# Performance work log

Hardware: AMD Instinct MI355X
Metric: run time of the kernel (lower is better)

Reference implementation:

```python
import jax, jax.numpy as jnp
import numpy as np

B = 65536
D = 512
R = 64  # min(64, D) reflections (cap_householder_refl=True)


def setup_inputs() -> dict:
    key = jax.random.key(0)
    k1, k2 = jax.random.split(key)
    x = jax.random.normal(k1, (B, D), dtype=jnp.float32)
    sldj = jnp.zeros((B,), dtype=jnp.float32)
    householder_params = jax.random.normal(k2, (D, R), dtype=jnp.float32)
    return {"x": x, "sldj": sldj, "householder_params": householder_params}


def reference(x, sldj, householder_params):
    # Sequential Householder reflections: x <- x - 2 (x . u_hat) u_hat
    # params: (D, R); unconditioned, so u is shared across the batch.
    us = householder_params.T  # (R, D), scanned in forward order i = 0..R-1

    def step(xc, u):
        unit_u = u / jnp.linalg.norm(u)          # (D,)
        scalar = xc @ unit_u                      # (B,)
        xc = xc - 2.0 * scalar[:, None] * unit_u  # rank-1 update
        return xc, None

    out, _ = jax.lax.scan(step, x, us)
    return out, sldj
```

## Files before the change

### kernel.cpp

```cpp
#include <hip/hip_runtime.h>

typedef __attribute__((ext_vector_type(8))) short bf16x8;
typedef __attribute__((ext_vector_type(4))) float f32x4;

#define DD 512
#define RR 64
#define BTOT 65536
#define BM 64
#define BK 32

static __device__ __forceinline__ unsigned short f2bf(float f) {
    union { float f; unsigned u; } v; v.f = f;
    unsigned r = v.u + 0x7fffu + ((v.u >> 16) & 1u);
    return (unsigned short)(r >> 16);
}

__global__ void normalize_kernel(const float* __restrict__ P, float* __restrict__ U) {
    int i = blockIdx.x;
    int t = threadIdx.x;
    __shared__ float red[4];
    float a = P[t * RR + i];
    float b = P[(t + 256) * RR + i];
    float p = a * a + b * b;
#pragma unroll
    for (int off = 32; off > 0; off >>= 1) p += __shfl_down(p, off);
    if ((t & 63) == 0) red[t >> 6] = p;
    __syncthreads();
    float s = red[0] + red[1] + red[2] + red[3];
    float inv = 1.0f / sqrtf(s);
    U[i * DD + t]       = a * inv;
    U[i * DD + t + 256] = b * inv;
}

__global__ void compose_kernel(const float* __restrict__ U, unsigned short* __restrict__ Mt) {
    int k = blockIdx.x;
    int t = threadIdx.x;
    __shared__ float red[4];
    float v0 = (k < 256 && t == k) ? 1.0f : 0.0f;
    float v1 = (k >= 256 && t == (k - 256)) ? 1.0f : 0.0f;
    for (int i = 0; i < RR; ++i) {
        float u0 = U[i * DD + t];
        float u1 = U[i * DD + t + 256];
        float p = v0 * u0 + v1 * u1;
#pragma unroll
        for (int off = 32; off > 0; off >>= 1) p += __shfl_down(p, off);
        if ((t & 63) == 0) red[t >> 6] = p;
        __syncthreads();
        float dot = red[0] + red[1] + red[2] + red[3];
        v0 -= 2.0f * dot * u0;
        v1 -= 2.0f * dot * u1;
        __syncthreads();
    }
    Mt[(size_t)t * DD + k]         = f2bf(v0);
    Mt[(size_t)(t + 256) * DD + k] = f2bf(v1);
}

__launch_bounds__(512, 4)
__global__ void gemm_kernel(const float* __restrict__ X,
                            const unsigned short* __restrict__ Mt,
                            float* __restrict__ out) {
    __shared__ __attribute__((aligned(16))) unsigned short lA[BM * BK];
    __shared__ __attribute__((aligned(16))) unsigned short lB[DD * BK];
    int t = threadIdx.x;
    int wave = t >> 6, lane = t & 63;
    int quad = lane >> 4, l16 = lane & 15;
    int row0 = blockIdx.x * BM;

    f32x4 acc[4][4] = {};

    int ar = t >> 3;
    int ak = (t & 7) * 4;
    const float* xrow = X + (size_t)(row0 + ar) * DD + ak;

    int bn_lane = lane >> 2;
    int bk_lane = (lane & 3) * 8;

    for (int k0 = 0; k0 < DD; k0 += BK) {
#pragma unroll
        for (int q = 0; q < 4; ++q) {
            int nbase = wave * 64 + q * 16;
            const unsigned short* g = Mt + (size_t)(nbase + bn_lane) * DD + k0 + bk_lane;
            __builtin_amdgcn_global_load_lds(
                (const __attribute__((address_space(1))) unsigned int*)g,
                (__attribute__((address_space(3))) unsigned int*)(lB + nbase * BK),
                16, 0, 0);
        }
        float4 xv = *(const float4*)(xrow + k0);
        ushort4 hv = make_ushort4(f2bf(xv.x), f2bf(xv.y), f2bf(xv.z), f2bf(xv.w));
        *(ushort4*)(lA + ar * BK + ak) = hv;
        __syncthreads();

        bf16x8 afr[4], bfr[4];
#pragma unroll
        for (int mt = 0; mt < 4; ++mt)
            afr[mt] = *(const bf16x8*)(lA + (mt * 16 + l16) * BK + quad * 8);
#pragma unroll
        for (int nt = 0; nt < 4; ++nt)
            bfr[nt] = *(const bf16x8*)(lB + (wave * 64 + nt * 16 + l16) * BK + quad * 8);
#pragma unroll
        for (int mt = 0; mt < 4; ++mt)
#pragma unroll
            for (int nt = 0; nt < 4; ++nt)
                acc[mt][nt] = __builtin_amdgcn_mfma_f32_16x16x32_bf16(afr[mt], bfr[nt], acc[mt][nt], 0, 0, 0);
        __syncthreads();
    }

#pragma unroll
    for (int mt = 0; mt < 4; ++mt) {
#pragma unroll
        for (int r = 0; r < 4; ++r) {
            int row = row0 + mt * 16 + quad * 4 + r;
            float* orow = out + (size_t)row * DD + wave * 64 + l16;
#pragma unroll
            for (int nt = 0; nt < 4; ++nt)
                orow[nt * 16] = acc[mt][nt][r];
        }
    }
}

__global__ void sldj_kernel(const float* __restrict__ s, float* __restrict__ o) {
    int i = blockIdx.x * blockDim.x + threadIdx.x;
    o[i] = s[i];
}

extern "C" void kernel_launch(void* const* d_in, const int* in_sizes, int n_in,
                              void* d_out, int out_size, void* d_ws, size_t ws_size,
                              hipStream_t stream) {
    const float* x      = (const float*)d_in[0];
    const float* sldj   = (const float*)d_in[1];
    const float* params = (const float*)d_in[2];
    float* out = (float*)d_out;

    float* U = (float*)d_ws;
    unsigned short* Mt = (unsigned short*)((char*)d_ws + RR * DD * sizeof(float));

    normalize_kernel<<<RR, 256, 0, stream>>>(params, U);
    compose_kernel<<<DD, 256, 0, stream>>>(U, Mt);
    gemm_kernel<<<BTOT / BM, 512, 0, stream>>>(x, Mt, out);
    sldj_kernel<<<BTOT / 256, 256, 0, stream>>>(sldj, out + (size_t)BTOT * DD);
}
```

Baseline: 326.8 us.

## Retile GEMM to 128x128 with async fp32 A loads and batch compose columns

The GEMM moves from 64-row blocks covering all 512 columns to 128x128 tiles on 4 waves. Both X (as fp32) and Mt are now loaded straight into LDS with global_load_lds, using XOR-swizzled layouts, and the bf16 conversion of A happens after the LDS read. The compose kernel now handles 4 columns per block, prefetches the next reflector and double-buffers the reduction slots so one barrier per step can be dropped. sldj copying is vectorised to float4. The new GEMM tiling re-reads each X tile four times, once per column tile, and converts A to bf16 redundantly across the two N-waves, but needs fewer registers per thread and avoids the synchronous global-load-then-convert step.

```diff
diff --git a/kernel.cpp b/kernel.cpp
--- a/kernel.cpp
+++ b/kernel.cpp
@@ -6,7 +6,8 @@
 #define DD 512
 #define RR 64
 #define BTOT 65536
-#define BM 64
+#define BM 128
+#define BN 128
 #define BK 32
 
 static __device__ __forceinline__ unsigned short f2bf(float f) {
@@ -33,75 +34,119 @@
 }
 
 __global__ void compose_kernel(const float* __restrict__ U, unsigned short* __restrict__ Mt) {
-    int k = blockIdx.x;
+    int kb = blockIdx.x * 4;
     int t = threadIdx.x;
-    __shared__ float red[4];
-    float v0 = (k < 256 && t == k) ? 1.0f : 0.0f;
-    float v1 = (k >= 256 && t == (k - 256)) ? 1.0f : 0.0f;
+    int w = t >> 6;
+    __shared__ float red[2][4][4];
+    float v0[4], v1[4];
+#pragma unroll
+    for (int c = 0; c < 4; ++c) {
+        v0[c] = (kb + c == t) ? 1.0f : 0.0f;
+        v1[c] = (kb + c == t + 256) ? 1.0f : 0.0f;
+    }
+    float u0n = U[t], u1n = U[t + 256];
     for (int i = 0; i < RR; ++i) {
-        float u0 = U[i * DD + t];
-        float u1 = U[i * DD + t + 256];
-        float p = v0 * u0 + v1 * u1;
+        float u0 = u0n, u1 = u1n;
+        if (i + 1 < RR) { u0n = U[(i + 1) * DD + t]; u1n = U[(i + 1) * DD + t + 256]; }
+        float p0 = v0[0] * u0 + v1[0] * u1;
+        float p1 = v0[1] * u0 + v1[1] * u1;
+        float p2 = v0[2] * u0 + v1[2] * u1;
+        float p3 = v0[3] * u0 + v1[3] * u1;
 #pragma unroll
-        for (int off = 32; off > 0; off >>= 1) p += __shfl_down(p, off);
-        if ((t & 63) == 0) red[t >> 6] = p;
+        for (int off = 32; off > 0; off >>= 1) {
+            p0 += __shfl_down(p0, off);
+            p1 += __shfl_down(p1, off);
+            p2 += __shfl_down(p2, off);
+            p3 += __shfl_down(p3, off);
+        }
+        if ((t & 63) == 0) {
+            red[i & 1][w][0] = p0; red[i & 1][w][1] = p1;
+            red[i & 1][w][2] = p2; red[i & 1][w][3] = p3;
+        }
         __syncthreads();
-        float dot = red[0] + red[1] + red[2] + red[3];
-        v0 -= 2.0f * dot * u0;
-        v1 -= 2.0f * dot * u1;
-        __syncthreads();
+        float d[4];
+#pragma unroll
+        for (int c = 0; c < 4; ++c)
+            d[c] = red[i & 1][0][c] + red[i & 1][1][c] + red[i & 1][2][c] + red[i & 1][3][c];
+#pragma unroll
+        for (int c = 0; c < 4; ++c) {
+            v0[c] -= 2.0f * d[c] * u0;
+            v1[c] -= 2.0f * d[c] * u1;
+        }
     }
-    Mt[(size_t)t * DD + k]         = f2bf(v0);
-    Mt[(size_t)(t + 256) * DD + k] = f2bf(v1);
+#pragma unroll
+    for (int c = 0; c < 4; ++c) {
+        Mt[(size_t)t * DD + kb + c]         = f2bf(v0[c]);
+        Mt[(size_t)(t + 256) * DD + kb + c] = f2bf(v1[c]);
+    }
 }
 
-__launch_bounds__(512, 4)
+__launch_bounds__(256, 4)
 __global__ void gemm_kernel(const float* __restrict__ X,
                             const unsigned short* __restrict__ Mt,
                             float* __restrict__ out) {
-    __shared__ __attribute__((aligned(16))) unsigned short lA[BM * BK];
-    __shared__ __attribute__((aligned(16))) unsigned short lB[DD * BK];
+    __shared__ __attribute__((aligned(16))) float lAf[BM * BK];
+    __shared__ __attribute__((aligned(16))) unsigned short lB[BN * BK];
+
     int t = threadIdx.x;
     int wave = t >> 6, lane = t & 63;
+    int wm = wave >> 1, wn = wave & 1;
     int quad = lane >> 4, l16 = lane & 15;
-    int row0 = blockIdx.x * BM;
+    int row0 = (int)(blockIdx.x >> 2) * BM;
+    int col0 = (int)(blockIdx.x & 3) * BN;
 
     f32x4 acc[4][4] = {};
 
-    int ar = t >> 3;
-    int ak = (t & 7) * 4;
-    const float* xrow = X + (size_t)(row0 + ar) * DD + ak;
+    int a_kg = (lane & 7) ^ (lane >> 3);
+    int a_mrow = wave * 32 + (lane >> 3);
+    int b_kg = (lane & 3) ^ ((lane >> 2) & 3);
+    int b_nrow = wave * 32 + (lane >> 2);
 
-    int bn_lane = lane >> 2;
-    int bk_lane = (lane & 3) * 8;
+    const float* aBase = X + (size_t)(row0 + a_mrow) * DD + a_kg * 4;
+    const unsigned short* bBase = Mt + (size_t)(col0 + b_nrow) * DD + b_kg * 8;
 
+#pragma unroll 1
     for (int k0 = 0; k0 < DD; k0 += BK) {
 #pragma unroll
         for (int q = 0; q < 4; ++q) {
-            int nbase = wave * 64 + q * 16;
-            const unsigned short* g = Mt + (size_t)(nbase + bn_lane) * DD + k0 + bk_lane;
+            const float* g = aBase + k0 + (size_t)q * 8 * DD;
             __builtin_amdgcn_global_load_lds(
                 (const __attribute__((address_space(1))) unsigned int*)g,
-                (__attribute__((address_space(3))) unsigned int*)(lB + nbase * BK),
+                (__attribute__((address_space(3))) unsigned int*)(lAf + (wave * 32 + q * 8) * BK),
                 16, 0, 0);
         }
-        float4 xv = *(const float4*)(xrow + k0);
-        ushort4 hv = make_ushort4(f2bf(xv.x), f2bf(xv.y), f2bf(xv.z), f2bf(xv.w));
-        *(ushort4*)(lA + ar * BK + ak) = hv;
+#pragma unroll
+        for (int q = 0; q < 2; ++q) {
+            const unsigned short* g = bBase + k0 + (size_t)q * 16 * DD;
+            __builtin_amdgcn_global_load_lds(
+                (const __attribute__((address_space(1))) unsigned int*)g,
+                (__attribute__((address_space(3))) unsigned int*)(lB + (wave * 32 + q * 16) * BK),
+                16, 0, 0);
+        }
         __syncthreads();
 
-        bf16x8 afr[4], bfr[4];
+        bf16x8 bfr[4];
 #pragma unroll
-        for (int mt = 0; mt < 4; ++mt)
-            afr[mt] = *(const bf16x8*)(lA + (mt * 16 + l16) * BK + quad * 8);
+        for (int nt = 0; nt < 4; ++nt) {
+            int n = wn * 64 + nt * 16 + l16;
+            bfr[nt] = *(const bf16x8*)(lB + n * BK + (quad ^ (l16 & 3)) * 8);
+        }
 #pragma unroll
-        for (int nt = 0; nt < 4; ++nt)
-            bfr[nt] = *(const bf16x8*)(lB + (wave * 64 + nt * 16 + l16) * BK + quad * 8);
-#pragma unroll
-        for (int mt = 0; mt < 4; ++mt)
+        for (int mt = 0; mt < 4; ++mt) {
+            int m = wm * 64 + mt * 16 + l16;
+            int s0 = (2 * quad) ^ (l16 & 7);
+            int s1 = (2 * quad + 1) ^ (l16 & 7);
+            float4 fa0 = *(const float4*)(lAf + m * BK + s0 * 4);
+            float4 fa1 = *(const float4*)(lAf + m * BK + s1 * 4);
+            bf16x8 afr;
+            afr[0] = (short)f2bf(fa0.x); afr[1] = (short)f2bf(fa0.y);
+            afr[2] = (short)f2bf(fa0.z); afr[3] = (short)f2bf(fa0.w);
+            afr[4] = (short)f2bf(fa1.x); afr[5] = (short)f2bf(fa1.y);
+            afr[6] = (short)f2bf(fa1.z); afr[7] = (short)f2bf(fa1.w);
 #pragma unroll
             for (int nt = 0; nt < 4; ++nt)
-                acc[mt][nt] = __builtin_amdgcn_mfma_f32_16x16x32_bf16(afr[mt], bfr[nt], acc[mt][nt], 0, 0, 0);
+                acc[mt][nt] = __builtin_amdgcn_mfma_f32_16x16x32_bf16(afr, bfr[nt], acc[mt][nt], 0, 0, 0);
+        }
         __syncthreads();
     }
 
@@ -109,8 +154,8 @@
     for (int mt = 0; mt < 4; ++mt) {
 #pragma unroll
         for (int r = 0; r < 4; ++r) {
-            int row = row0 + mt * 16 + quad * 4 + r;
-            float* orow = out + (size_t)row * DD + wave * 64 + l16;
+            int row = row0 + wm * 64 + mt * 16 + quad * 4 + r;
+            float* orow = out + (size_t)row * DD + col0 + wn * 64 + l16;
 #pragma unroll
             for (int nt = 0; nt < 4; ++nt)
                 orow[nt * 16] = acc[mt][nt][r];
@@ -118,7 +163,7 @@
     }
 }
 
-__global__ void sldj_kernel(const float* __restrict__ s, float* __restrict__ o) {
+__global__ void sldj_kernel(const float4* __restrict__ s, float4* __restrict__ o) {
     int i = blockIdx.x * blockDim.x + threadIdx.x;
     o[i] = s[i];
 }
@@ -135,7 +180,8 @@
     unsigned short* Mt = (unsigned short*)((char*)d_ws + RR * DD * sizeof(float));
 
     normalize_kernel<<<RR, 256, 0, stream>>>(params, U);
-    compose_kernel<<<DD, 256, 0, stream>>>(U, Mt);
-    gemm_kernel<<<BTOT / BM, 512, 0, stream>>>(x, Mt, out);
-    sldj_kernel<<<BTOT / 256, 256, 0, stream>>>(sldj, out + (size_t)BTOT * DD);
+    compose_kernel<<<DD / 4, 256, 0, stream>>>(U, Mt);
+    gemm_kernel<<<(BTOT / BM) * (DD / BN), 256, 0, stream>>>(x, Mt, out);
+    sldj_kernel<<<BTOT / 4 / 256, 256, 0, stream>>>((const float4*)sldj,
+                                                    (float4*)(out + (size_t)BTOT * DD));
 }
```

Measured after the change: 304.2 us. -6.9%, faster.
